# Performance work log

Measured on AMD Instinct MI355X. Metric: run time of the kernel, lower is better.

The kernel has to match this reference:

```python
import jax, jax.numpy as jnp
import numpy as np
import math

B, LQ, LK, D = 8, 128, 256, 32
ET, H, NH = 32, 8, 64
ETK = ET // H  # 4
LN_EPS = 1e-5


def setup_inputs() -> dict:
    key = jax.random.key(0)
    ks = jax.random.split(key, 12)
    s = 0.02
    return {
        "query_tt": jax.random.uniform(ks[0], (B, LQ), jnp.float32),
        "key_tt": jax.random.uniform(ks[1], (B, LK), jnp.float32),
        "value": jax.random.normal(ks[2], (B, LK, D), jnp.float32),
        "emb_mask": jax.random.randint(ks[3], (B, LK, D), 0, 2, jnp.int32),
        "w_time": jax.random.normal(ks[4], (1, 1), jnp.float32) * s,
        "b_time": jnp.zeros((1,), jnp.float32),
        "w_periodic": jax.random.normal(ks[5], (ET - 1,), jnp.float32) * s,
        "b_periodic": jnp.zeros((ET - 1,), jnp.float32),
        "w_decay": jnp.array([[0.1]], jnp.float32),
        "vt_w1": jax.random.normal(ks[6], (D, NH), jnp.float32) * s,
        "vt_b1": jnp.zeros((NH,), jnp.float32),
        "ln_g": jnp.ones((NH,), jnp.float32),
        "ln_b": jnp.zeros((NH,), jnp.float32),
        "vt_w2": jax.random.normal(ks[7], (NH, D), jnp.float32) * s,
        "vt_b2": jnp.zeros((D,), jnp.float32),
        "wq": jax.random.normal(ks[8], (ET, ET), jnp.float32) * s,
        "bq": jnp.zeros((ET,), jnp.float32),
        "wk": jax.random.normal(ks[9], (ET, ET), jnp.float32) * s,
        "bk": jnp.zeros((ET,), jnp.float32),
        "wo": jax.random.normal(ks[10], (H * D, NH), jnp.float32) * s,
        "bo": jnp.zeros((NH,), jnp.float32),
    }


def _forward(query_tt, key_tt, value, emb_mask, w_time, b_time, w_periodic, b_periodic,
             w_decay, vt_w1, vt_b1, ln_g, ln_b, vt_w2, vt_b2, wq, bq, wk, bk, wo, bo):
    Bv, Lq = query_tt.shape
    Lk = key_tt.shape[1]
    Dv = value.shape[-1]

    # ---- value transfer embedding ----
    v = jnp.broadcast_to(value[:, None, :, :], (Bv, Lq, Lk, Dv))  # [B,Lq,Lk,D]
    d_t = query_tt[:, :, None] - key_tt[:, None, :]               # [B,Lq,Lk]
    hdn = v @ vt_w1 + vt_b1                                       # [B,Lq,Lk,NH]
    mu = hdn.mean(-1, keepdims=True)
    var = ((hdn - mu) ** 2).mean(-1, keepdims=True)
    hdn = (hdn - mu) * jax.lax.rsqrt(var + LN_EPS) * ln_g + ln_b  # LayerNorm
    hdn = jax.nn.relu(hdn)
    d_value = hdn @ vt_w2 + vt_b2                                 # [B,Lq,Lk,D]
    dt1 = d_t[..., None]                                          # [B,Lq,Lk,1]
    time_decay = 1.0 / (1.0 + dt1 * w_decay[0, 0])
    v = d_value * time_decay * dt1 + v                            # [B,Lq,Lk,D]

    # ---- learned time embedding ----
    def time_emb(tt):
        t = tt[..., None]  # [B,L,1]
        return jnp.concatenate([t * w_time[0, 0] + b_time,
                                jnp.sin(t * w_periodic + b_periodic)], axis=-1)  # [B,L,ET]

    q = (time_emb(query_tt) @ wq + bq).reshape(Bv, Lq, H, ETK).transpose(0, 2, 1, 3)  # [B,h,Lq,etk]
    k = (time_emb(key_tt) @ wk + bk).reshape(Bv, Lk, H, ETK).transpose(0, 2, 1, 3)    # [B,h,Lk,etk]

    # ---- per-value-dim attention ----
    scores = jnp.einsum('bhqe,bhke->bhqk', q, k) / math.sqrt(ETK)          # [B,h,Lq,Lk]
    mask5 = emb_mask[:, None, None, :, :]                                   # [B,1,1,Lk,D]
    scores5 = jnp.where(mask5 == 0, jnp.float32(-10000.0), scores[..., None])  # [B,h,Lq,Lk,D]
    p_attn = jax.nn.softmax(scores5, axis=-2)                               # softmax over Lk, per dim d
    x = jnp.einsum('bhqkd,bqkd->bhqd', p_attn, v)                           # [B,h,Lq,D]
    x = x.transpose(0, 2, 1, 3).reshape(Bv, Lq, H * Dv)
    return x @ wo + bo                                                      # [B,Lq,NH]


def reference(query_tt, key_tt, value, emb_mask, w_time, b_time, w_periodic, b_periodic,
              w_decay, vt_w1, vt_b1, ln_g, ln_b, vt_w2, vt_b2, wq, bq, wk, bk, wo, bo):
    return _forward(query_tt, key_tt, value, emb_mask, w_time, b_time, w_periodic, b_periodic,
                    w_decay, vt_w1, vt_b1, ln_g, ln_b, vt_w2, vt_b2, wq, bq, wk, bk, wo, bo)
```

## Files before the change

kernel.cpp:

```cpp
#include <hip/hip_runtime.h>

#define Bv_ 8
#define LQ 128
#define LK 256
#define Dv 32
#define ET 32
#define Hh 8
#define NH 64
#define PADK 257

__global__ __launch_bounds__(256) void prep_kernel(
    const float* __restrict__ qtt, const float* __restrict__ ktt,
    const float* __restrict__ value, const int* __restrict__ emb_mask,
    const float* __restrict__ w_time, const float* __restrict__ b_time,
    const float* __restrict__ w_per, const float* __restrict__ b_per,
    const float* __restrict__ vt_w1, const float* __restrict__ vt_b1,
    const float* __restrict__ ln_g, const float* __restrict__ ln_b,
    const float* __restrict__ vt_w2, const float* __restrict__ vt_b2,
    const float* __restrict__ wq, const float* __restrict__ bq,
    const float* __restrict__ wk, const float* __restrict__ bk,
    float* __restrict__ A, float* __restrict__ Bdv, float* __restrict__ mf,
    float* __restrict__ qe, float* __restrict__ ke)
{
    const int t = threadIdx.x;
    const int blk = blockIdx.x;

    if (blk < 512) {
        __shared__ float vrow[4][Dv];
        __shared__ float hrow[4][NH];
        const int w = t >> 6;
        const int l = t & 63;
        const int row = blk * 4 + w;

        if (l < Dv) vrow[w][l] = value[row * Dv + l];
        __syncthreads();

        float h = vt_b1[l];
        #pragma unroll
        for (int d = 0; d < Dv; ++d) h += vrow[w][d] * vt_w1[d * NH + l];

        float s = h;
        #pragma unroll
        for (int off = 32; off > 0; off >>= 1) s += __shfl_xor(s, off);
        const float mu = s * (1.0f / NH);
        const float dc = h - mu;
        float vs = dc * dc;
        #pragma unroll
        for (int off = 32; off > 0; off >>= 1) vs += __shfl_xor(vs, off);
        const float rs = rsqrtf(vs * (1.0f / NH) + 1e-5f);
        float hn = dc * rs * ln_g[l] + ln_b[l];
        hrow[w][l] = fmaxf(hn, 0.0f);
        __syncthreads();

        if (l < Dv) {
            float dval = vt_b2[l];
            #pragma unroll
            for (int j = 0; j < NH; ++j) dval += hrow[w][j] * vt_w2[j * Dv + l];
            const float mm = (emb_mask[row * Dv + l] != 0) ? 1.0f : 0.0f;
            A[row * Dv + l]   = mm * vrow[w][l];
            Bdv[row * Dv + l] = mm * dval;
            mf[row * Dv + l]  = mm;
        }
    } else {
        const int idx = blk - 512;
        const int sub = t >> 5;
        const int j = t & 31;
        const int row = idx * 8 + sub;
        __shared__ float eb[8][ET];

        float tt;
        const float *W, *bias;
        float* outp;
        if (row < Bv_ * LQ) {
            tt = qtt[row];
            W = wq; bias = bq; outp = qe + row * ET;
        } else {
            const int r2 = row - Bv_ * LQ;
            tt = ktt[r2];
            W = wk; bias = bk; outp = ke + r2 * ET;
        }
        float e;
        if (j == 0) e = tt * w_time[0] + b_time[0];
        else        e = __sinf(tt * w_per[j - 1] + b_per[j - 1]);
        eb[sub][j] = e;
        __syncthreads();

        float o = bias[j];
        #pragma unroll
        for (int i = 0; i < ET; ++i) o += eb[sub][i] * W[i * ET + j];
        outp[j] = o;
    }
}

__global__ __launch_bounds__(256, 1) void attn_kernel(
    const float* __restrict__ qtt, const float* __restrict__ ktt,
    const float* __restrict__ w_decay,
    const float* __restrict__ A, const float* __restrict__ Bdv,
    const float* __restrict__ mf,
    const float* __restrict__ qe, const float* __restrict__ ke,
    const float* __restrict__ wo, const float* __restrict__ bo,
    float* __restrict__ out)
{
    __shared__ float As[LK * Dv];
    __shared__ float Bs[LK * Dv];
    __shared__ float Ms[LK * Dv];
    __shared__ float Esh[4 * Hh * PADK];
    __shared__ float Gsh[4 * LK];
    __shared__ float qrow_s[4 * ET];
    __shared__ float4 xsh4[4 * 64];

    const int t = threadIdx.x;
    const int blk = blockIdx.x;
    const int b = blk >> 5;
    const int q0 = (blk & 31) * 4;

    {
        const float4* Ag = (const float4*)(A   + (size_t)b * LK * Dv);
        const float4* Bg = (const float4*)(Bdv + (size_t)b * LK * Dv);
        const float4* Mg = (const float4*)(mf  + (size_t)b * LK * Dv);
        float4* As4 = (float4*)As;
        float4* Bs4 = (float4*)Bs;
        float4* Ms4 = (float4*)Ms;
        #pragma unroll
        for (int i = 0; i < 8; ++i) {
            const int idx = i * 256 + t;
            As4[idx] = Ag[idx];
            Bs4[idx] = Bg[idx];
            Ms4[idx] = Mg[idx];
        }
    }
    if (t < 4 * ET) qrow_s[t] = qe[((size_t)b * LQ + q0) * ET + t];
    __syncthreads();

    {
        const int k = t;
        const float4* kerow = (const float4*)(ke + ((size_t)b * LK + k) * ET);
        float4 kreg[Hh];
        #pragma unroll
        for (int h = 0; h < Hh; ++h) kreg[h] = kerow[h];
        const float ktime = ktt[b * LK + k];
        const float wd = w_decay[0];
        #pragma unroll
        for (int q = 0; q < 4; ++q) {
            const float dt = qtt[b * LQ + q0 + q] - ktime;
            Gsh[q * LK + k] = dt / fmaf(wd, dt, 1.0f);
            const float4* qq4 = (const float4*)(qrow_s + q * ET);
            #pragma unroll
            for (int h = 0; h < Hh; ++h) {
                const float4 qq = qq4[h];
                const float4 kv = kreg[h];
                const float sc = 0.5f * (qq.x * kv.x + qq.y * kv.y +
                                         qq.z * kv.z + qq.w * kv.w);
                Esh[(q * Hh + h) * PADK + k] = __expf(sc);
            }
        }
    }
    __syncthreads();

    const int ks = t >> 6;
    const int h  = (t >> 3) & 7;
    const int d4 = t & 7;
    float4 accN[4], accD[4];
    #pragma unroll
    for (int q = 0; q < 4; ++q) {
        accN[q] = make_float4(0.f, 0.f, 0.f, 0.f);
        accD[q] = make_float4(0.f, 0.f, 0.f, 0.f);
    }
    {
        const float4* As4 = (const float4*)As;
        const float4* Bs4 = (const float4*)Bs;
        const float4* Ms4 = (const float4*)Ms;
        const float* Eh0 = Esh + h * PADK;
        const int k0 = ks * 64;
        #pragma unroll 4
        for (int kk_ = 0; kk_ < 64; ++kk_) {
            const int k = k0 + kk_;
            const float4 a  = As4[k * 8 + d4];
            const float4 bb = Bs4[k * 8 + d4];
            const float4 m  = Ms4[k * 8 + d4];
            #pragma unroll
            for (int q = 0; q < 4; ++q) {
                const float e  = Eh0[q * (Hh * PADK) + k];
                const float eg = e * Gsh[q * LK + k];
                accN[q].x = fmaf(e, a.x, fmaf(eg, bb.x, accN[q].x));
                accN[q].y = fmaf(e, a.y, fmaf(eg, bb.y, accN[q].y));
                accN[q].z = fmaf(e, a.z, fmaf(eg, bb.z, accN[q].z));
                accN[q].w = fmaf(e, a.w, fmaf(eg, bb.w, accN[q].w));
                accD[q].x = fmaf(e, m.x, accD[q].x);
                accD[q].y = fmaf(e, m.y, accD[q].y);
                accD[q].z = fmaf(e, m.z, accD[q].z);
                accD[q].w = fmaf(e, m.w, accD[q].w);
            }
        }
    }
    __syncthreads();

    {
        float4* psN = (float4*)As;
        float4* psD = ((float4*)As) + 1024;
        const int cls = t & 63;
        #pragma unroll
        for (int q = 0; q < 4; ++q) {
            psN[(ks * 4 + q) * 64 + cls] = accN[q];
            psD[(ks * 4 + q) * 64 + cls] = accD[q];
        }
    }
    __syncthreads();

    {
        const int q = t >> 6, cls = t & 63;
        const float4* psN = (const float4*)As;
        const float4* psD = ((const float4*)As) + 1024;
        float4 n = make_float4(0.f, 0.f, 0.f, 0.f);
        float4 d = make_float4(0.f, 0.f, 0.f, 0.f);
        #pragma unroll
        for (int s = 0; s < 4; ++s) {
            const float4 nn = psN[(s * 4 + q) * 64 + cls];
            const float4 dd = psD[(s * 4 + q) * 64 + cls];
            n.x += nn.x; n.y += nn.y; n.z += nn.z; n.w += nn.w;
            d.x += dd.x; d.y += dd.y; d.z += dd.z; d.w += dd.w;
        }
        float4 x;
        x.x = n.x / fmaxf(d.x, 1e-30f);
        x.y = n.y / fmaxf(d.y, 1e-30f);
        x.z = n.z / fmaxf(d.z, 1e-30f);
        x.w = n.w / fmaxf(d.w, 1e-30f);
        xsh4[q * 64 + cls] = x;
    }
    __syncthreads();

    {
        const int q = t >> 6, j = t & 63;
        float acc = bo[j];
        #pragma unroll 8
        for (int c4 = 0; c4 < 64; ++c4) {
            const float4 xv = xsh4[q * 64 + c4];
            const int c = c4 * 4;
            acc = fmaf(xv.x, wo[(c + 0) * NH + j], acc);
            acc = fmaf(xv.y, wo[(c + 1) * NH + j], acc);
            acc = fmaf(xv.z, wo[(c + 2) * NH + j], acc);
            acc = fmaf(xv.w, wo[(c + 3) * NH + j], acc);
        }
        out[((size_t)b * LQ + q0 + q) * NH + j] = acc;
    }
}

extern "C" void kernel_launch(void* const* d_in, const int* in_sizes, int n_in,
                              void* d_out, int out_size, void* d_ws, size_t ws_size,
                              hipStream_t stream) {
    const float* qtt      = (const float*)d_in[0];
    const float* ktt      = (const float*)d_in[1];
    const float* value    = (const float*)d_in[2];
    const int*   emb_mask = (const int*)  d_in[3];
    const float* w_time   = (const float*)d_in[4];
    const float* b_time   = (const float*)d_in[5];
    const float* w_per    = (const float*)d_in[6];
    const float* b_per    = (const float*)d_in[7];
    const float* w_decay  = (const float*)d_in[8];
    const float* vt_w1    = (const float*)d_in[9];
    const float* vt_b1    = (const float*)d_in[10];
    const float* ln_g     = (const float*)d_in[11];
    const float* ln_b     = (const float*)d_in[12];
    const float* vt_w2    = (const float*)d_in[13];
    const float* vt_b2    = (const float*)d_in[14];
    const float* wq       = (const float*)d_in[15];
    const float* bq       = (const float*)d_in[16];
    const float* wk       = (const float*)d_in[17];
    const float* bk       = (const float*)d_in[18];
    const float* wo       = (const float*)d_in[19];
    const float* bo       = (const float*)d_in[20];
    float* out = (float*)d_out;

    float* ws  = (float*)d_ws;
    float* Aw  = ws;
    float* Bw  = ws + 65536;
    float* Mw  = ws + 131072;
    float* qew = ws + 196608;
    float* kew = ws + 229376;

    hipLaunchKernelGGL(prep_kernel, dim3(896), dim3(256), 0, stream,
                       qtt, ktt, value, emb_mask, w_time, b_time, w_per, b_per,
                       vt_w1, vt_b1, ln_g, ln_b, vt_w2, vt_b2,
                       wq, bq, wk, bk, Aw, Bw, Mw, qew, kew);

    hipLaunchKernelGGL(attn_kernel, dim3(256), dim3(256), 0, stream,
                       qtt, ktt, w_decay, Aw, Bw, Mw, qew, kew, wo, bo, out);
}
```

Baseline: 114.6 us.

## Pack attention operands as fp16 pairs and accumulate with packed dot2

The prep kernel now writes A, masked d_value and mask as fp16 pairs interleaving adjacent key rows, which halves workspace traffic and LDS footprint. The attention kernel stores exp scores and exp*decay weights as fp16 and uses the fdot2 instruction to process two keys per op. The main loop is re-tiled so each thread handles two heads, four queries, four dims and a 32-key slice, followed by an 8-way LDS reduction. This cuts FMA count and LDS loads, at the cost of fp16 rounding of the softmax weights and values, which may hurt accuracy.

```diff
diff --git a/kernel.cpp b/kernel.cpp
--- a/kernel.cpp
+++ b/kernel.cpp
@@ -7,7 +7,27 @@
 #define ET 32
 #define Hh 8
 #define NH 64
-#define PADK 257
+
+typedef __fp16 h2 __attribute__((ext_vector_type(2)));
+
+static __device__ __forceinline__ h2 bch(unsigned u) {
+    union { unsigned u; h2 h; } c; c.u = u; return c.h;
+}
+static __device__ __forceinline__ unsigned pack2(float lo, float hi) {
+    union { h2 h; unsigned u; } c;
+    c.h = __builtin_amdgcn_cvt_pkrtz(lo, hi);
+    return c.u;
+}
+static __device__ __forceinline__ unsigned short h16(float x) {
+    union { __fp16 h; unsigned short u; } c; c.h = (__fp16)x; return c.u;
+}
+static __device__ __forceinline__ float dot2(h2 a, h2 b, float c) {
+#if __has_builtin(__builtin_amdgcn_fdot2)
+    return __builtin_amdgcn_fdot2(a, b, c, false);
+#else
+    return fmaf((float)a.x, (float)b.x, fmaf((float)a.y, (float)b.y, c));
+#endif
+}
 
 __global__ __launch_bounds__(256) void prep_kernel(
     const float* __restrict__ qtt, const float* __restrict__ ktt,
@@ -19,7 +39,8 @@
     const float* __restrict__ vt_w2, const float* __restrict__ vt_b2,
     const float* __restrict__ wq, const float* __restrict__ bq,
     const float* __restrict__ wk, const float* __restrict__ bk,
-    float* __restrict__ A, float* __restrict__ Bdv, float* __restrict__ mf,
+    unsigned* __restrict__ A2g, unsigned* __restrict__ B2g,
+    unsigned* __restrict__ M2g,
     float* __restrict__ qe, float* __restrict__ ke)
 {
     const int t = threadIdx.x;
@@ -28,6 +49,7 @@
     if (blk < 512) {
         __shared__ float vrow[4][Dv];
         __shared__ float hrow[4][NH];
+        __shared__ float sha[4][Dv], shb[4][Dv], shm[4][Dv];
         const int w = t >> 6;
         const int l = t & 63;
         const int row = blk * 4 + w;
@@ -48,8 +70,7 @@
         #pragma unroll
         for (int off = 32; off > 0; off >>= 1) vs += __shfl_xor(vs, off);
         const float rs = rsqrtf(vs * (1.0f / NH) + 1e-5f);
-        float hn = dc * rs * ln_g[l] + ln_b[l];
-        hrow[w][l] = fmaxf(hn, 0.0f);
+        hrow[w][l] = fmaxf(dc * rs * ln_g[l] + ln_b[l], 0.0f);
         __syncthreads();
 
         if (l < Dv) {
@@ -57,9 +78,22 @@
             #pragma unroll
             for (int j = 0; j < NH; ++j) dval += hrow[w][j] * vt_w2[j * Dv + l];
             const float mm = (emb_mask[row * Dv + l] != 0) ? 1.0f : 0.0f;
-            A[row * Dv + l]   = mm * vrow[w][l];
-            Bdv[row * Dv + l] = mm * dval;
-            mf[row * Dv + l]  = mm;
+            sha[w][l] = mm * vrow[w][l];
+            shb[w][l] = mm * dval;
+            shm[w][l] = mm;
+        }
+        __syncthreads();
+
+        if (t < 192) {
+            const int arr = t >> 6;
+            const int pr  = (t >> 5) & 1;
+            const int d   = t & 31;
+            float lo, hi;
+            unsigned* dst;
+            if (arr == 0)      { lo = sha[2*pr][d]; hi = sha[2*pr+1][d]; dst = A2g; }
+            else if (arr == 1) { lo = shb[2*pr][d]; hi = shb[2*pr+1][d]; dst = B2g; }
+            else               { lo = shm[2*pr][d]; hi = shm[2*pr+1][d]; dst = M2g; }
+            dst[(blk * 2 + pr) * 32 + d] = pack2(lo, hi);
         }
     } else {
         const int idx = blk - 512;
@@ -72,12 +106,10 @@
         const float *W, *bias;
         float* outp;
         if (row < Bv_ * LQ) {
-            tt = qtt[row];
-            W = wq; bias = bq; outp = qe + row * ET;
+            tt = qtt[row]; W = wq; bias = bq; outp = qe + row * ET;
         } else {
             const int r2 = row - Bv_ * LQ;
-            tt = ktt[r2];
-            W = wk; bias = bk; outp = ke + r2 * ET;
+            tt = ktt[r2]; W = wk; bias = bk; outp = ke + r2 * ET;
         }
         float e;
         if (j == 0) e = tt * w_time[0] + b_time[0];
@@ -95,19 +127,22 @@
 __global__ __launch_bounds__(256, 1) void attn_kernel(
     const float* __restrict__ qtt, const float* __restrict__ ktt,
     const float* __restrict__ w_decay,
-    const float* __restrict__ A, const float* __restrict__ Bdv,
-    const float* __restrict__ mf,
+    const unsigned* __restrict__ A2g, const unsigned* __restrict__ B2g,
+    const unsigned* __restrict__ M2g,
     const float* __restrict__ qe, const float* __restrict__ ke,
     const float* __restrict__ wo, const float* __restrict__ bo,
     float* __restrict__ out)
 {
-    __shared__ float As[LK * Dv];
-    __shared__ float Bs[LK * Dv];
-    __shared__ float Ms[LK * Dv];
-    __shared__ float Esh[4 * Hh * PADK];
-    __shared__ float Gsh[4 * LK];
-    __shared__ float qrow_s[4 * ET];
-    __shared__ float4 xsh4[4 * 64];
+    __shared__ __align__(16) unsigned LDSu[31364];
+    unsigned* A2s = LDSu;
+    unsigned* B2s = LDSu + 4096;
+    unsigned* M2s = LDSu + 8192;
+    float*    kes = (float*)(LDSu + 12288);
+    unsigned* E2s  = LDSu + 21760;
+    unsigned* EG2s = LDSu + 25984;
+    float*    qrs = (float*)(LDSu + 30208);
+    float*    XSH = (float*)(LDSu + 30336);
+    float*    qts = (float*)(LDSu + 31360);
 
     const int t = threadIdx.x;
     const int blk = blockIdx.x;
@@ -115,108 +150,126 @@
     const int q0 = (blk & 31) * 4;
 
     {
-        const float4* Ag = (const float4*)(A   + (size_t)b * LK * Dv);
-        const float4* Bg = (const float4*)(Bdv + (size_t)b * LK * Dv);
-        const float4* Mg = (const float4*)(mf  + (size_t)b * LK * Dv);
-        float4* As4 = (float4*)As;
-        float4* Bs4 = (float4*)Bs;
-        float4* Ms4 = (float4*)Ms;
+        const uint4* Ag = (const uint4*)(A2g + (size_t)b * 4096);
+        const uint4* Bg = (const uint4*)(B2g + (size_t)b * 4096);
+        const uint4* Mg = (const uint4*)(M2g + (size_t)b * 4096);
+        #pragma unroll
+        for (int i = 0; i < 4; ++i) {
+            const int idx = i * 256 + t;
+            ((uint4*)A2s)[idx] = Ag[idx];
+            ((uint4*)B2s)[idx] = Bg[idx];
+            ((uint4*)M2s)[idx] = Mg[idx];
+        }
+        const float4* keg = (const float4*)(ke + (size_t)b * LK * ET);
         #pragma unroll
         for (int i = 0; i < 8; ++i) {
             const int idx = i * 256 + t;
-            As4[idx] = Ag[idx];
-            Bs4[idx] = Bg[idx];
-            Ms4[idx] = Mg[idx];
-        }
-    }
-    if (t < 4 * ET) qrow_s[t] = qe[((size_t)b * LQ + q0) * ET + t];
-    __syncthreads();
-
-    {
-        const int k = t;
-        const float4* kerow = (const float4*)(ke + ((size_t)b * LK + k) * ET);
-        float4 kreg[Hh];
-        #pragma unroll
-        for (int h = 0; h < Hh; ++h) kreg[h] = kerow[h];
-        const float ktime = ktt[b * LK + k];
+            const int row = idx >> 3, c = idx & 7;
+            *(float4*)&kes[row * 37 + c * 4] = keg[idx];
+        }
+        if (t < 128) qrs[t] = 0.5f * qe[((size_t)b * LQ + q0) * ET + t];
+        if (t < 4)   qts[t] = qtt[b * LQ + q0 + t];
+    }
+    __syncthreads();
+
+    {
+        const float ktk = ktt[b * LK + t];
         const float wd = w_decay[0];
+        unsigned short* E2u  = (unsigned short*)E2s;
+        unsigned short* EG2u = (unsigned short*)EG2s;
+        float4 kr[8];
+        #pragma unroll
+        for (int h = 0; h < 8; ++h) kr[h] = *(const float4*)&kes[t * 37 + h * 4];
         #pragma unroll
         for (int q = 0; q < 4; ++q) {
-            const float dt = qtt[b * LQ + q0 + q] - ktime;
-            Gsh[q * LK + k] = dt / fmaf(wd, dt, 1.0f);
-            const float4* qq4 = (const float4*)(qrow_s + q * ET);
-            #pragma unroll
-            for (int h = 0; h < Hh; ++h) {
-                const float4 qq = qq4[h];
-                const float4 kv = kreg[h];
-                const float sc = 0.5f * (qq.x * kv.x + qq.y * kv.y +
-                                         qq.z * kv.z + qq.w * kv.w);
-                Esh[(q * Hh + h) * PADK + k] = __expf(sc);
+            const float dt = qts[q] - ktk;
+            const float g = dt / fmaf(wd, dt, 1.0f);
+            #pragma unroll
+            for (int h = 0; h < 8; ++h) {
+                const float4 qq = *(const float4*)&qrs[q * 32 + h * 4];
+                float sc = qq.x * kr[h].x;
+                sc = fmaf(qq.y, kr[h].y, sc);
+                sc = fmaf(qq.z, kr[h].z, sc);
+                sc = fmaf(qq.w, kr[h].w, sc);
+                const float e = __expf(sc);
+                E2u[(q * 8 + h) * 264 + t]  = h16(e);
+                EG2u[(q * 8 + h) * 264 + t] = h16(e * g);
             }
         }
     }
     __syncthreads();
 
-    const int ks = t >> 6;
-    const int h  = (t >> 3) & 7;
-    const int d4 = t & 7;
-    float4 accN[4], accD[4];
+    const int ks = t >> 5, hg = (t >> 3) & 3, dg = t & 7;
+    const int hb = 2 * hg;
+    float accN[4][2][4] = {{{0}}}, accD[4][2][4] = {{{0}}};
+    {
+        const unsigned* Eb  = E2s  + ks * 16;
+        const unsigned* EGb = EG2s + ks * 16;
+        const unsigned* Ab = A2s + ks * 512 + dg * 4;
+        const unsigned* Bb = B2s + ks * 512 + dg * 4;
+        const unsigned* Mb = M2s + ks * 512 + dg * 4;
+        #pragma unroll
+        for (int si = 0; si < 4; ++si) {
+            unsigned eu[4][2][4], egu[4][2][4];
+            unsigned au[4][4], bu[4][4], mu_[4][4];
+            #pragma unroll
+            for (int q = 0; q < 4; ++q) {
+                #pragma unroll
+                for (int hh = 0; hh < 2; ++hh) {
+                    const uint4 v = *(const uint4*)(Eb  + (q*8 + hb + hh)*132 + si*4);
+                    const uint4 w = *(const uint4*)(EGb + (q*8 + hb + hh)*132 + si*4);
+                    eu[q][hh][0]=v.x; eu[q][hh][1]=v.y; eu[q][hh][2]=v.z; eu[q][hh][3]=v.w;
+                    egu[q][hh][0]=w.x; egu[q][hh][1]=w.y; egu[q][hh][2]=w.z; egu[q][hh][3]=w.w;
+                }
+            }
+            #pragma unroll
+            for (int j = 0; j < 4; ++j) {
+                const uint4 a  = *(const uint4*)(Ab + (si*4 + j)*32);
+                const uint4 bb = *(const uint4*)(Bb + (si*4 + j)*32);
+                const uint4 m  = *(const uint4*)(Mb + (si*4 + j)*32);
+                au[j][0]=a.x; au[j][1]=a.y; au[j][2]=a.z; au[j][3]=a.w;
+                bu[j][0]=bb.x; bu[j][1]=bb.y; bu[j][2]=bb.z; bu[j][3]=bb.w;
+                mu_[j][0]=m.x; mu_[j][1]=m.y; mu_[j][2]=m.z; mu_[j][3]=m.w;
+            }
+            #pragma unroll
+            for (int q = 0; q < 4; ++q)
+            #pragma unroll
+            for (int hh = 0; hh < 2; ++hh)
+            #pragma unroll
+            for (int j = 0; j < 4; ++j) {
+                const h2 e2  = bch(eu[q][hh][j]);
+                const h2 eg2 = bch(egu[q][hh][j]);
+                #pragma unroll
+                for (int dd = 0; dd < 4; ++dd) {
+                    accN[q][hh][dd] = dot2(e2,  bch(au[j][dd]),  accN[q][hh][dd]);
+                    accN[q][hh][dd] = dot2(eg2, bch(bu[j][dd]),  accN[q][hh][dd]);
+                    accD[q][hh][dd] = dot2(e2,  bch(mu_[j][dd]), accD[q][hh][dd]);
+                }
+            }
+        }
+    }
+    __syncthreads();
+
+    float* REDN = kes;
+    float* REDD = (float*)LDSu;
     #pragma unroll
-    for (int q = 0; q < 4; ++q) {
-        accN[q] = make_float4(0.f, 0.f, 0.f, 0.f);
-        accD[q] = make_float4(0.f, 0.f, 0.f, 0.f);
-    }
-    {
-        const float4* As4 = (const float4*)As;
-        const float4* Bs4 = (const float4*)Bs;
-        const float4* Ms4 = (const float4*)Ms;
-        const float* Eh0 = Esh + h * PADK;
-        const int k0 = ks * 64;
-        #pragma unroll 4
-        for (int kk_ = 0; kk_ < 64; ++kk_) {
-            const int k = k0 + kk_;
-            const float4 a  = As4[k * 8 + d4];
-            const float4 bb = Bs4[k * 8 + d4];
-            const float4 m  = Ms4[k * 8 + d4];
-            #pragma unroll
-            for (int q = 0; q < 4; ++q) {
-                const float e  = Eh0[q * (Hh * PADK) + k];
-                const float eg = e * Gsh[q * LK + k];
-                accN[q].x = fmaf(e, a.x, fmaf(eg, bb.x, accN[q].x));
-                accN[q].y = fmaf(e, a.y, fmaf(eg, bb.y, accN[q].y));
-                accN[q].z = fmaf(e, a.z, fmaf(eg, bb.z, accN[q].z));
-                accN[q].w = fmaf(e, a.w, fmaf(eg, bb.w, accN[q].w));
-                accD[q].x = fmaf(e, m.x, accD[q].x);
-                accD[q].y = fmaf(e, m.y, accD[q].y);
-                accD[q].z = fmaf(e, m.z, accD[q].z);
-                accD[q].w = fmaf(e, m.w, accD[q].w);
-            }
-        }
-    }
-    __syncthreads();
-
-    {
-        float4* psN = (float4*)As;
-        float4* psD = ((float4*)As) + 1024;
-        const int cls = t & 63;
-        #pragma unroll
-        for (int q = 0; q < 4; ++q) {
-            psN[(ks * 4 + q) * 64 + cls] = accN[q];
-            psD[(ks * 4 + q) * 64 + cls] = accD[q];
-        }
-    }
-    __syncthreads();
-
-    {
-        const int q = t >> 6, cls = t & 63;
-        const float4* psN = (const float4*)As;
-        const float4* psD = ((const float4*)As) + 1024;
-        float4 n = make_float4(0.f, 0.f, 0.f, 0.f);
-        float4 d = make_float4(0.f, 0.f, 0.f, 0.f);
-        #pragma unroll
-        for (int s = 0; s < 4; ++s) {
-            const float4 nn = psN[(s * 4 + q) * 64 + cls];
-            const float4 dd = psD[(s * 4 + q) * 64 + cls];
+    for (int q = 0; q < 4; ++q)
+    #pragma unroll
+    for (int hh = 0; hh < 2; ++hh) {
+        const int c = (q * 8 + hb + hh) * 32 + dg * 4;
+        *(float4*)&REDN[ks * 1024 + c] =
+            make_float4(accN[q][hh][0], accN[q][hh][1], accN[q][hh][2], accN[q][hh][3]);
+        *(float4*)&REDD[ks * 1024 + c] =
+            make_float4(accD[q][hh][0], accD[q][hh][1], accD[q][hh][2], accD[q][hh][3]);
+    }
+    __syncthreads();
+
+    {
+        float4 n = make_float4(0.f,0.f,0.f,0.f), d = make_float4(0.f,0.f,0.f,0.f);
+        #pragma unroll
+        for (int s = 0; s < 8; ++s) {
+            const float4 nn = *(const float4*)&REDN[s * 1024 + t * 4];
+            const float4 dd = *(const float4*)&REDD[s * 1024 + t * 4];
             n.x += nn.x; n.y += nn.y; n.z += nn.z; n.w += nn.w;
             d.x += dd.x; d.y += dd.y; d.z += dd.z; d.w += dd.w;
         }
@@ -225,16 +278,17 @@
         x.y = n.y / fmaxf(d.y, 1e-30f);
         x.z = n.z / fmaxf(d.z, 1e-30f);
         x.w = n.w / fmaxf(d.w, 1e-30f);
-        xsh4[q * 64 + cls] = x;
+        *(float4*)&XSH[t * 4] = x;
     }
     __syncthreads();
 
     {
         const int q = t >> 6, j = t & 63;
         float acc = bo[j];
+        const float4* xq = (const float4*)&XSH[q * 256];
         #pragma unroll 8
         for (int c4 = 0; c4 < 64; ++c4) {
-            const float4 xv = xsh4[q * 64 + c4];
+            const float4 xv = xq[c4];
             const int c = c4 * 4;
             acc = fmaf(xv.x, wo[(c + 0) * NH + j], acc);
             acc = fmaf(xv.y, wo[(c + 1) * NH + j], acc);
@@ -271,18 +325,18 @@
     const float* bo       = (const float*)d_in[20];
     float* out = (float*)d_out;
 
-    float* ws  = (float*)d_ws;
-    float* Aw  = ws;
-    float* Bw  = ws + 65536;
-    float* Mw  = ws + 131072;
-    float* qew = ws + 196608;
-    float* kew = ws + 229376;
+    unsigned* wsu = (unsigned*)d_ws;
+    unsigned* A2g = wsu;
+    unsigned* B2g = wsu + 32768;
+    unsigned* M2g = wsu + 65536;
+    float*    qew = (float*)(wsu + 98304);
+    float*    kew = (float*)(wsu + 131072);
 
     hipLaunchKernelGGL(prep_kernel, dim3(896), dim3(256), 0, stream,
                        qtt, ktt, value, emb_mask, w_time, b_time, w_per, b_per,
                        vt_w1, vt_b1, ln_g, ln_b, vt_w2, vt_b2,
-                       wq, bq, wk, bk, Aw, Bw, Mw, qew, kew);
+                       wq, bq, wk, bk, A2g, B2g, M2g, qew, kew);
 
     hipLaunchKernelGGL(attn_kernel, dim3(256), dim3(256), 0, stream,
-                       qtt, ktt, w_decay, Aw, Bw, Mw, qew, kew, wo, bo, out);
-}
+                       qtt, ktt, w_decay, A2g, B2g, M2g, qew, kew, wo, bo, out);
+}
```

After: 112.7 us. No clear change (-1.7%).
